# Performance work log

Measured on AMD Instinct MI355X. Metric: run time of the kernel, lower is better.

The kernel has to match this reference:

```python
import jax, jax.numpy as jnp
import numpy as np
from jax import lax

DWT_SCALE = 0.5
IDWT_SCALE = 1.0
PAD = 2  # (kernel_size-1)//2 for k=5


def haar_dwt(x, s):
    """x: [B,C,H,W] -> (ll, lh, hl, hh) each [B,C,H/2,W/2]. 2x2 Haar, scale s."""
    a = x[..., 0::2, 0::2]
    b = x[..., 0::2, 1::2]
    c = x[..., 1::2, 0::2]
    d = x[..., 1::2, 1::2]
    ll = s * (a + b + c + d)
    lh = s * (a + b - c - d)
    hl = s * (a - b + c - d)
    hh = s * (a - b - c + d)
    return ll, lh, hl, hh


def haar_idwt(ll, lh, hl, hh, s):
    """Inverse of haar_dwt when s_dwt * s_idwt_total = 0.5. Returns [B,C,2H,2W]."""
    a = s * (ll + lh + hl + hh)
    b = s * (ll + lh - hl - hh)
    c = s * (ll - lh + hl - hh)
    d = s * (ll - lh - hl + hh)
    B, C, H2, W2 = ll.shape
    top = jnp.stack([a, b], axis=-1).reshape(B, C, H2, 2 * W2)  # even rows
    bot = jnp.stack([c, d], axis=-1).reshape(B, C, H2, 2 * W2)  # odd rows
    return jnp.stack([top, bot], axis=-2).reshape(B, C, 2 * H2, 2 * W2)


def conv2d(x, w, pad):
    return lax.conv_general_dilated(
        x, w, window_strides=(1, 1), padding=[(pad, pad), (pad, pad)],
        dimension_numbers=("NCHW", "OIHW", "NCHW"))


def setup_inputs() -> dict:
    key = jax.random.key(0)
    kx, k0, k1, k2, kb = jax.random.split(key, 5)
    C, K = 64, 5
    x = jax.random.normal(kx, (8, C, 256, 256), dtype=jnp.float32)
    # kaiming_uniform-ish small init to keep 3-level recursion numerically tame
    scale = 0.02
    w0 = jax.random.normal(k0, (4 * C, 4 * C, K, K), dtype=jnp.float32) * scale
    w1 = jax.random.normal(k1, (4 * C, 4 * C, K, K), dtype=jnp.float32) * scale
    w2 = jax.random.normal(k2, (4 * C, 4 * C, K, K), dtype=jnp.float32) * scale
    bias = jax.random.normal(kb, (C,), dtype=jnp.float32) * 0.01
    return {"x": x, "w0": w0, "w1": w1, "w2": w2, "bias": bias}


def reference(x, w0, w1, w2, bias):
    weights = [w0, w1, w2]
    idwt_s = DWT_SCALE * IDWT_SCALE  # perfect reconstruction pair
    curr = x
    ll_levels, high_levels = [], []
    for w in weights:
        ll, lh, hl, hh = haar_dwt(curr, DWT_SCALE)
        curr = ll  # pre-conv LL feeds the next level
        B, C, H2, W2 = ll.shape
        stacked = jnp.stack([ll, lh, hl, hh], axis=2).reshape(B, 4 * C, H2, W2)
        y = conv2d(stacked, w, PAD)  # [B, 4*Co, H2, W2]
        y = y.reshape(B, -1, 4, H2, W2)
        ll_levels.append(y[:, :, 0])
        high_levels.append(y[:, :, 1:])
    next_ll = jnp.zeros_like(ll_levels[-1])
    for ll_t, h_t in zip(reversed(ll_levels), reversed(high_levels)):
        ll = ll_t + next_ll
        next_ll = haar_idwt(ll, h_t[:, :, 0], h_t[:, :, 1], h_t[:, :, 2], idwt_s)
    return next_ll + bias.reshape(1, -1, 1, 1)
```

## Files before the change

kernel.cpp:

```cpp
#include <hip/hip_runtime.h>


typedef unsigned short u16;
typedef __attribute__((ext_vector_type(8))) __bf16 bf16x8;
typedef __attribute__((ext_vector_type(4))) float f32x4;

__device__ __forceinline__ u16 f2bf(float f) {
  union { float f; unsigned u; } v; v.f = f;
  unsigned r = v.u + 0x7fffu + ((v.u >> 16) & 1u);
  return (u16)(r >> 16);
}
__device__ __forceinline__ float bf2f(u16 u) {
  union { unsigned u; float f; } v; v.u = ((unsigned)u) << 16;
  return v.f;
}

typedef const unsigned int __attribute__((address_space(1)))* gas1_t;
typedef unsigned int __attribute__((address_space(3)))* gas3_t;
__device__ __forceinline__ void gload16(const void* g, void* l) {
  __builtin_amdgcn_global_load_lds((gas1_t)g, (gas3_t)l, 16, 0, 0);
}

__global__ void k_wtrans(const float* __restrict__ w, u16* __restrict__ wb) {
  int co = blockIdx.x;
  int ci = threadIdx.x;
  const float* src = w + ((long)co * 256 + ci) * 25;
  float v[25];
#pragma unroll
  for (int tp = 0; tp < 25; ++tp) v[tp] = src[tp];
#pragma unroll
  for (int tp = 0; tp < 25; ++tp)
    wb[((long)tp * 256 + co) * 256 + ci] = f2bf(v[tp]);
}

__global__ void k_border(u16* __restrict__ st, int B_, int H2, int W2) {
  int PW = W2 + 4;
  int npix = 4 * PW + 4 * H2;
  int gid = blockIdx.x * blockDim.x + threadIdx.x;
  int pid = gid >> 6, lane = gid & 63;
  if (pid >= B_ * npix) return;
  int b = pid / npix, p = pid % npix;
  int row, col;
  if (p < 2 * PW) { row = p / PW; col = p % PW; }
  else if (p < 4 * PW) { int q = p - 2 * PW; row = H2 + 2 + q / PW; col = q % PW; }
  else { int q = p - 4 * PW; row = 2 + (q >> 2); int c4 = q & 3; col = (c4 < 2) ? c4 : W2 + c4; }
  long base = (((long)b * (H2 + 4) + row) * PW + col) * 256 + lane * 4;
  *(ushort4*)(st + base) = make_ushort4(0, 0, 0, 0);
}

__global__ void k_dwt(const float* __restrict__ in, u16* __restrict__ st,
                      float* __restrict__ ll, int B_, int H2, int W2) {
  int idx = blockIdx.x * blockDim.x + threadIdx.x;
  int W2h = W2 >> 1;
  int total = B_ * 64 * H2 * W2h;
  if (idx >= total) return;
  int w2h = idx % W2h; int t2 = idx / W2h;
  int h2 = t2 % H2; t2 /= H2;
  int c = t2 % 64; int b = t2 / 64;
  int w2 = w2h * 2;
  const float* r0 = in + (((long)(b * 64 + c) * (2 * H2) + 2 * h2) * (2 * W2)) + 2 * w2;
  const float* r1 = r0 + 2 * W2;
  float4 tp = *(const float4*)r0;
  float4 bt = *(const float4*)r1;
  float ll0 = 0.5f * (tp.x + tp.y + bt.x + bt.y);
  float lh0 = 0.5f * (tp.x + tp.y - bt.x - bt.y);
  float hl0 = 0.5f * (tp.x - tp.y + bt.x - bt.y);
  float hh0 = 0.5f * (tp.x - tp.y - bt.x + bt.y);
  float ll1 = 0.5f * (tp.z + tp.w + bt.z + bt.w);
  float lh1 = 0.5f * (tp.z + tp.w - bt.z - bt.w);
  float hl1 = 0.5f * (tp.z - tp.w + bt.z - bt.w);
  float hh1 = 0.5f * (tp.z - tp.w - bt.z + bt.w);
  long sbase = (((long)b * (H2 + 4) + (h2 + 2)) * (W2 + 4) + (w2 + 2)) * 256 + 4 * c;
  *(ushort4*)(st + sbase)       = make_ushort4(f2bf(ll0), f2bf(lh0), f2bf(hl0), f2bf(hh0));
  *(ushort4*)(st + sbase + 256) = make_ushort4(f2bf(ll1), f2bf(lh1), f2bf(hl1), f2bf(hh1));
  long lbase = (((long)(b * 64 + c) * H2) + h2) * W2 + w2;
  *(float2*)(ll + lbase) = make_float2(ll0, ll1);
}

__global__ __launch_bounds__(512, 2) void k_conv8(
    const u16* __restrict__ st, const u16* __restrict__ wt, u16* __restrict__ out,
    int H2, int W2, int ktot, int nsplit) {
  __shared__ __align__(16) char smem[131072];
  const int t = threadIdx.x;
  const int lane = t & 63;
  const int wv = t >> 6;
  const int wm = wv >> 2, wn = wv & 3;
  const int nwg = gridDim.x;
  const int bid = blockIdx.x;
  const int lb = (bid & 7) * (nwg >> 3) + (bid >> 3);
  const int m0 = lb * 256;
  const int PW = W2 + 4;
  const int spl = blockIdx.y;
  const int kk0 = (spl * ktot) / nsplit;
  const int kk1 = ((spl + 1) * ktot) / nsplit;
  const long Mrows = (long)nwg * 256;
  u16* yo = out + (long)spl * Mrows * 256;

  const int trow = t >> 3;
  const int srcci = ((t & 7) ^ (trow & 7)) * 8;
  const char* baseA[4];
#pragma unroll
  for (int u = 0; u < 4; ++u) {
    int m = m0 + u * 64 + trow;
    int w = m % W2; int q = m / W2;
    int hh = q % H2; int b = q / H2;
    long sp = ((long)(b * (H2 + 4) + hh + 2) * PW + (w + 2));
    baseA[u] = (const char*)(st + sp * 256 + srcci);
  }
  const char* baseB0 = (const char*)(wt + trow * 256 + srcci);

  f32x4 acc[8][4];
#pragma unroll
  for (int i = 0; i < 8; ++i)
#pragma unroll
    for (int j = 0; j < 4; ++j) acc[i][j] = f32x4{0.f, 0.f, 0.f, 0.f};

  const int kq = (lane >> 4) * 16;
  const int sw = (lane & 7) << 4;
  int va0 = (wm * 128 + (lane & 15)) * 128 + (kq ^ sw);
  int va1 = (wm * 128 + (lane & 15)) * 128 + ((64 + kq) ^ sw);
  int vb0 = 32768 + (wn * 64 + (lane & 15)) * 128 + (kq ^ sw);
  int vb1 = 32768 + (wn * 64 + (lane & 15)) * 128 + ((64 + kq) ^ sw);

  bf16x8 a0[4][2], a1[4][2], b0[2][2], b1[2][2];

  auto offsets = [&](int kk, long& oA, long& oB) {
    int tap = kk >> 2, cic = kk & 3;
    int dy = tap / 5 - 2, dx = tap % 5 - 2;
    oA = ((long)(dy * PW + dx) * 256 + cic * 64) * 2;
    oB = ((long)tap * 65536 + cic * 64) * 2;
  };
  auto stageA4 = [&](long off, int dsto) {
    char* d = smem + dsto + wv * 1024;
#pragma unroll
    for (int u = 0; u < 4; ++u) gload16(baseA[u] + off, d + u * 8192);
  };
  auto stageB4 = [&](long off, int dsto) {
    char* d = smem + dsto + 32768 + wv * 1024;
#pragma unroll
    for (int u = 0; u < 4; ++u) gload16(baseB0 + u * 32768 + off, d + u * 8192);
  };

#define LDA0 { _Pragma("unroll") for (int i = 0; i < 4; ++i) {       \
    a0[i][0] = *(const bf16x8*)(smem + va0 + i * 2048);              \
    a0[i][1] = *(const bf16x8*)(smem + va1 + i * 2048); } }
#define LDA1 { _Pragma("unroll") for (int i = 0; i < 4; ++i) {       \
    a1[i][0] = *(const bf16x8*)(smem + va0 + 8192 + i * 2048);       \
    a1[i][1] = *(const bf16x8*)(smem + va1 + 8192 + i * 2048); } }
#define LDB0 { _Pragma("unroll") for (int j = 0; j < 2; ++j) {       \
    b0[j][0] = *(const bf16x8*)(smem + vb0 + j * 2048);              \
    b0[j][1] = *(const bf16x8*)(smem + vb1 + j * 2048); } }
#define LDB1 { _Pragma("unroll") for (int j = 0; j < 2; ++j) {       \
    b1[j][0] = *(const bf16x8*)(smem + vb0 + 4096 + j * 2048);       \
    b1[j][1] = *(const bf16x8*)(smem + vb1 + 4096 + j * 2048); } }
#define MMQ(A, B, IB, JB)                                                     \
  _Pragma("unroll") for (int i = 0; i < 4; ++i)                               \
  _Pragma("unroll") for (int j = 0; j < 2; ++j)                               \
  _Pragma("unroll") for (int k = 0; k < 2; ++k)                               \
    acc[(IB) + i][(JB) + j] = __builtin_amdgcn_mfma_f32_16x16x32_bf16(        \
        A[i][k], B[j][k], acc[(IB) + i][(JB) + j], 0, 0, 0);

  long oA, oB;
  offsets(kk0, oA, oB);
  stageA4(oA, 0); stageB4(oB, 0);
  offsets(kk0 + 1, oA, oB);
  stageA4(oA, 65536); stageB4(oB, 65536);
  asm volatile("s_waitcnt vmcnt(8)" ::: "memory");
  __builtin_amdgcn_s_barrier();
  LDA0 LDB0

  int curo = 0;
  for (int kt = kk0; kt < kk1; ++kt) {
    const bool stg = (kt + 2) < kk1;
    const bool rd1 = (kt + 1) < kk1;
    LDA1 LDB1
    va0 ^= 65536; va1 ^= 65536; vb0 ^= 65536; vb1 ^= 65536;
    __builtin_amdgcn_s_barrier();
    asm volatile("s_waitcnt lgkmcnt(12)" ::: "memory");
    __builtin_amdgcn_sched_barrier(0);
    __builtin_amdgcn_s_setprio(1);
    MMQ(a0, b0, 0, 0)
    __builtin_amdgcn_s_setprio(0);
    __builtin_amdgcn_s_barrier();
    asm volatile("s_waitcnt lgkmcnt(4)" ::: "memory");
    __builtin_amdgcn_sched_barrier(0);
    __builtin_amdgcn_s_setprio(1);
    MMQ(a1, b0, 4, 0)
    __builtin_amdgcn_s_setprio(0);
    if (rd1) { asm volatile("s_waitcnt vmcnt(0)" ::: "memory"); }
    __builtin_amdgcn_s_barrier();
    asm volatile("s_waitcnt lgkmcnt(0)" ::: "memory");
    __builtin_amdgcn_sched_barrier(0);
    __builtin_amdgcn_s_setprio(1);
    MMQ(a1, b1, 4, 2)
    __builtin_amdgcn_s_setprio(0);
    if (rd1) { LDB0 }
    if (stg) { offsets(kt + 2, oA, oB); stageA4(oA, curo); }
    __builtin_amdgcn_s_barrier();
    __builtin_amdgcn_s_setprio(1);
    MMQ(a0, b1, 0, 2)
    __builtin_amdgcn_s_setprio(0);
    if (stg) { stageB4(oB, curo); }
    if (rd1) { LDA0 }
    curo ^= 65536;
  }
#undef MMQ
#undef LDA0
#undef LDA1
#undef LDB0
#undef LDB1

#pragma unroll
  for (int i = 0; i < 8; ++i) {
    int mloc = m0 + wm * 128 + i * 16 + (lane >> 4) * 4;
#pragma unroll
    for (int j = 0; j < 4; ++j) {
      int nloc = wn * 64 + j * 16 + (lane & 15);
#pragma unroll
      for (int r = 0; r < 4; ++r)
        yo[(long)(mloc + r) * 256 + nloc] = f2bf(acc[i][j][r]);
    }
  }
}

__global__ void k_red(const u16* __restrict__ p, u16* __restrict__ y, long n, int ns) {
  long i = ((long)blockIdx.x * 256 + threadIdx.x) * 4;
  if (i >= n) return;
  float s0 = 0.f, s1 = 0.f, s2 = 0.f, s3 = 0.f;
  for (int k = 0; k < ns; ++k) {
    ushort4 v = *(const ushort4*)(p + (long)k * n + i);
    s0 += bf2f(v.x); s1 += bf2f(v.y); s2 += bf2f(v.z); s3 += bf2f(v.w);
  }
  *(ushort4*)(y + i) = make_ushort4(f2bf(s0), f2bf(s1), f2bf(s2), f2bf(s3));
}

__global__ void k_idwt(const u16* __restrict__ y, const float* __restrict__ nll,
                       float* __restrict__ out, const float* __restrict__ bias,
                       int B_, int H2, int W2) {
  int idx = blockIdx.x * blockDim.x + threadIdx.x;
  int W2h = W2 >> 1;
  int total = B_ * 64 * H2 * W2h;
  if (idx >= total) return;
  int w2h = idx % W2h; int t2 = idx / W2h;
  int h2 = t2 % H2; t2 /= H2;
  int c = t2 % 64; int b = t2 / 64;
  int w2 = w2h * 2;
  long ybase = (((long)b * H2 + h2) * W2 + w2) * 256 + 4 * c;
  ushort4 q0 = *(const ushort4*)(y + ybase);
  ushort4 q1 = *(const ushort4*)(y + ybase + 256);
  float llv0 = bf2f(q0.x), lh0 = bf2f(q0.y), hl0 = bf2f(q0.z), hh0 = bf2f(q0.w);
  float llv1 = bf2f(q1.x), lh1 = bf2f(q1.y), hl1 = bf2f(q1.z), hh1 = bf2f(q1.w);
  if (nll) {
    float2 nv = *(const float2*)(nll + (((long)(b * 64 + c) * H2 + h2) * W2 + w2));
    llv0 += nv.x; llv1 += nv.y;
  }
  float bv = bias ? bias[c] : 0.f;
  float a0 = 0.5f * (llv0 + lh0 + hl0 + hh0) + bv;
  float b0 = 0.5f * (llv0 + lh0 - hl0 - hh0) + bv;
  float c0 = 0.5f * (llv0 - lh0 + hl0 - hh0) + bv;
  float d0 = 0.5f * (llv0 - lh0 - hl0 + hh0) + bv;
  float a1 = 0.5f * (llv1 + lh1 + hl1 + hh1) + bv;
  float b1 = 0.5f * (llv1 + lh1 - hl1 - hh1) + bv;
  float c1 = 0.5f * (llv1 - lh1 + hl1 - hh1) + bv;
  float d1 = 0.5f * (llv1 - lh1 - hl1 + hh1) + bv;
  long obase = (((long)(b * 64 + c) * (2 * H2) + 2 * h2) * (2 * W2)) + 2 * w2;
  *(float4*)(out + obase)          = make_float4(a0, b0, a1, b1);
  *(float4*)(out + obase + 2 * W2) = make_float4(c0, d0, c1, d1);
}

constexpr size_t WBF_SZ1 = 25ull * 256 * 256 * 2;
constexpr size_t OFF_WBF = 0;
constexpr size_t OFF_S0  = 3 * WBF_SZ1;
constexpr size_t S0_SZ   = 8ull * 132 * 132 * 256 * 2;
constexpr size_t REL_S1 = 0;
constexpr size_t S1_SZ  = 8ull * 68 * 68 * 256 * 2;
constexpr size_t REL_L1 = REL_S1 + S1_SZ;
constexpr size_t L1_SZ  = 8ull * 64 * 64 * 64 * 4;
constexpr size_t REL_S2 = REL_L1 + L1_SZ;
constexpr size_t S2_SZ  = 8ull * 36 * 36 * 256 * 2;
constexpr size_t REL_Y1 = REL_S2 + S2_SZ;
constexpr size_t Y1_SZ  = 8ull * 64 * 64 * 256 * 2;
constexpr size_t REL_Y2 = REL_Y1 + Y1_SZ;
constexpr size_t Y2_SZ  = 8ull * 32 * 32 * 256 * 2;
constexpr size_t REL_N2 = REL_Y2 + Y2_SZ;
constexpr size_t N2_SZ  = 8ull * 64 * 64 * 64 * 4;
constexpr size_t REL_L2 = REL_N2 + N2_SZ;
constexpr size_t OFF_L0 = OFF_S0 + S0_SZ;
constexpr size_t OFF_Y0 = OFF_L0 + 8ull * 64 * 128 * 128 * 4;

extern "C" void kernel_launch(void* const* d_in, const int* in_sizes, int n_in,
                              void* d_out, int out_size, void* d_ws, size_t ws_size,
                              hipStream_t stream) {
  const float* x    = (const float*)d_in[0];
  const float* w0   = (const float*)d_in[1];
  const float* w1   = (const float*)d_in[2];
  const float* w2   = (const float*)d_in[3];
  const float* bias = (const float*)d_in[4];
  float* out = (float*)d_out;
  char* ws = (char*)d_ws;

  u16* wbf0 = (u16*)(ws + OFF_WBF);
  u16* wbf1 = (u16*)(ws + OFF_WBF + WBF_SZ1);
  u16* wbf2 = (u16*)(ws + OFF_WBF + 2 * WBF_SZ1);
  u16* s0 = (u16*)(ws + OFF_S0);
  u16* s1 = (u16*)(ws + OFF_S0 + REL_S1);
  float* l1 = (float*)(ws + OFF_S0 + REL_L1);
  u16* s2 = (u16*)(ws + OFF_S0 + REL_S2);
  u16* y1 = (u16*)(ws + OFF_S0 + REL_Y1);
  u16* y2 = (u16*)(ws + OFF_S0 + REL_Y2);
  float* n2 = (float*)(ws + OFF_S0 + REL_N2);
  float* l2 = (float*)(ws + OFF_S0 + REL_L2);
  float* l0 = (float*)(ws + OFF_L0);
  u16* P   = (u16*)(ws + OFF_L0);
  float* n1 = (float*)(ws + OFF_L0);
  u16* y0 = (u16*)(ws + OFF_Y0);

  k_wtrans<<<256, 256, 0, stream>>>(w0, wbf0);
  k_wtrans<<<256, 256, 0, stream>>>(w1, wbf1);
  k_wtrans<<<256, 256, 0, stream>>>(w2, wbf2);

  k_border<<<2080, 256, 0, stream>>>(s0, 8, 128, 128);
  k_dwt<<<16384, 256, 0, stream>>>(x, s0, l0, 8, 128, 128);
  k_conv8<<<dim3(512, 1), 512, 0, stream>>>(s0, wbf0, y0, 128, 128, 100, 1);

  k_border<<<1056, 256, 0, stream>>>(s1, 8, 64, 64);
  k_border<<<544, 256, 0, stream>>>(s2, 8, 32, 32);

  k_dwt<<<4096, 256, 0, stream>>>(l0, s1, l1, 8, 64, 64);
  k_conv8<<<dim3(128, 2), 512, 0, stream>>>(s1, wbf1, P, 64, 64, 100, 2);
  k_red<<<8192, 256, 0, stream>>>(P, y1, 8388608L, 2);

  k_dwt<<<1024, 256, 0, stream>>>(l1, s2, l2, 8, 32, 32);
  k_conv8<<<dim3(32, 8), 512, 0, stream>>>(s2, wbf2, P, 32, 32, 100, 8);
  k_red<<<2048, 256, 0, stream>>>(P, y2, 2097152L, 8);

  k_idwt<<<1024, 256, 0, stream>>>(y2, nullptr, n2, nullptr, 8, 32, 32);
  k_idwt<<<4096, 256, 0, stream>>>(y1, n2, n1, nullptr, 8, 64, 64);
  k_idwt<<<16384, 256, 0, stream>>>(y0, n1, out, bias, 8, 128, 128);
}
```

Baseline: 632.7 us.

## Fuse split-K reduction into IDWT, coalesce DWT/IDWT via LDS, merge weight transposes

Folds the split-K partial-sum reduction kernels into the inverse-DWT kernels, dropping the intermediate y1/y2 buffers and two launches. The DWT and IDWT kernels are restructured so each block handles a row segment across all channels, staging channel-interleaved bf16 data in LDS to get coalesced 16-byte global accesses. The three weight-transpose launches are merged into one grid. The workspace layout is reshuffled to reuse buffers, which risks aliasing if lifetimes overlap.

Measured after the change: 721.2 us. +14.0%, slower.

```diff
diff --git a/kernel.cpp b/kernel.cpp
--- a/kernel.cpp
+++ b/kernel.cpp
@@ -3,6 +3,7 @@
 
 typedef unsigned short u16;
 typedef __attribute__((ext_vector_type(8))) __bf16 bf16x8;
+typedef __attribute__((ext_vector_type(8))) unsigned short us8;
 typedef __attribute__((ext_vector_type(4))) float f32x4;
 
 __device__ __forceinline__ u16 f2bf(float f) {
@@ -21,7 +22,11 @@
   __builtin_amdgcn_global_load_lds((gas1_t)g, (gas3_t)l, 16, 0, 0);
 }
 
-__global__ void k_wtrans(const float* __restrict__ w, u16* __restrict__ wb) {
+__global__ void k_wtrans3(const float* __restrict__ wa, const float* __restrict__ wb_,
+                          const float* __restrict__ wc, u16* __restrict__ oa,
+                          u16* __restrict__ ob, u16* __restrict__ oc) {
+  const float* w = (blockIdx.y == 0) ? wa : (blockIdx.y == 1) ? wb_ : wc;
+  u16* o = (blockIdx.y == 0) ? oa : (blockIdx.y == 1) ? ob : oc;
   int co = blockIdx.x;
   int ci = threadIdx.x;
   const float* src = w + ((long)co * 256 + ci) * 25;
@@ -30,7 +35,7 @@
   for (int tp = 0; tp < 25; ++tp) v[tp] = src[tp];
 #pragma unroll
   for (int tp = 0; tp < 25; ++tp)
-    wb[((long)tp * 256 + co) * 256 + ci] = f2bf(v[tp]);
+    o[((long)tp * 256 + co) * 256 + ci] = f2bf(v[tp]);
 }
 
 __global__ void k_border(u16* __restrict__ st, int B_, int H2, int W2) {
@@ -48,33 +53,51 @@
   *(ushort4*)(st + base) = make_ushort4(0, 0, 0, 0);
 }
 
-__global__ void k_dwt(const float* __restrict__ in, u16* __restrict__ st,
-                      float* __restrict__ ll, int B_, int H2, int W2) {
-  int idx = blockIdx.x * blockDim.x + threadIdx.x;
-  int W2h = W2 >> 1;
-  int total = B_ * 64 * H2 * W2h;
-  if (idx >= total) return;
-  int w2h = idx % W2h; int t2 = idx / W2h;
-  int h2 = t2 % H2; t2 /= H2;
-  int c = t2 % 64; int b = t2 / 64;
-  int w2 = w2h * 2;
-  const float* r0 = in + (((long)(b * 64 + c) * (2 * H2) + 2 * h2) * (2 * W2)) + 2 * w2;
+template <int NCOLS>
+__global__ __launch_bounds__(256) void k_dwtT(const float* __restrict__ in,
+                                              u16* __restrict__ st, float* __restrict__ ll,
+                                              int B_, int H2, int W2, int nch) {
+  __shared__ u16 lds16[NCOLS * 256];
+  int blk = blockIdx.x;
+  int cw = blk % nch; int rest = blk / nch;
+  int h2 = rest % H2; int b = rest / H2;
+  int t = threadIdx.x;
+  int c = t >> 2, g = t & 3;
+  constexpr int NC4 = NCOLS / 4;
+  constexpr int NPAIR = NC4 / 2;
+
+  const float* r0 = in + (((long)(b * 64 + c) * (2 * H2) + 2 * h2) * (2 * W2)) + 2 * (cw * NCOLS + g * NC4);
   const float* r1 = r0 + 2 * W2;
-  float4 tp = *(const float4*)r0;
-  float4 bt = *(const float4*)r1;
-  float ll0 = 0.5f * (tp.x + tp.y + bt.x + bt.y);
-  float lh0 = 0.5f * (tp.x + tp.y - bt.x - bt.y);
-  float hl0 = 0.5f * (tp.x - tp.y + bt.x - bt.y);
-  float hh0 = 0.5f * (tp.x - tp.y - bt.x + bt.y);
-  float ll1 = 0.5f * (tp.z + tp.w + bt.z + bt.w);
-  float lh1 = 0.5f * (tp.z + tp.w - bt.z - bt.w);
-  float hl1 = 0.5f * (tp.z - tp.w + bt.z - bt.w);
-  float hh1 = 0.5f * (tp.z - tp.w - bt.z + bt.w);
-  long sbase = (((long)b * (H2 + 4) + (h2 + 2)) * (W2 + 4) + (w2 + 2)) * 256 + 4 * c;
-  *(ushort4*)(st + sbase)       = make_ushort4(f2bf(ll0), f2bf(lh0), f2bf(hl0), f2bf(hh0));
-  *(ushort4*)(st + sbase + 256) = make_ushort4(f2bf(ll1), f2bf(lh1), f2bf(hl1), f2bf(hh1));
-  long lbase = (((long)(b * 64 + c) * H2) + h2) * W2 + w2;
-  *(float2*)(ll + lbase) = make_float2(ll0, ll1);
+  float llv[NC4];
+#pragma unroll
+  for (int j = 0; j < NPAIR; ++j) {
+    float4 tp = *(const float4*)(r0 + 4 * j);
+    float4 bt = *(const float4*)(r1 + 4 * j);
+    float ll0 = 0.5f * (tp.x + tp.y + bt.x + bt.y);
+    float lh0 = 0.5f * (tp.x + tp.y - bt.x - bt.y);
+    float hl0 = 0.5f * (tp.x - tp.y + bt.x - bt.y);
+    float hh0 = 0.5f * (tp.x - tp.y - bt.x + bt.y);
+    float ll1 = 0.5f * (tp.z + tp.w + bt.z + bt.w);
+    float lh1 = 0.5f * (tp.z + tp.w - bt.z - bt.w);
+    float hl1 = 0.5f * (tp.z - tp.w + bt.z - bt.w);
+    float hh1 = 0.5f * (tp.z - tp.w - bt.z + bt.w);
+    int w = g * NC4 + 2 * j;
+    *(ushort4*)(lds16 + w * 256 + 4 * c)       = make_ushort4(f2bf(ll0), f2bf(lh0), f2bf(hl0), f2bf(hh0));
+    *(ushort4*)(lds16 + (w + 1) * 256 + 4 * c) = make_ushort4(f2bf(ll1), f2bf(lh1), f2bf(hl1), f2bf(hh1));
+    llv[2 * j] = ll0; llv[2 * j + 1] = ll1;
+  }
+  float* lp = ll + (((long)(b * 64 + c) * H2 + h2) * W2 + cw * NCOLS + g * NC4);
+#pragma unroll
+  for (int j = 0; j < NC4; j += 4)
+    *(float4*)(lp + j) = make_float4(llv[j], llv[j + 1], llv[j + 2], llv[j + 3]);
+  __syncthreads();
+  u16* dst = st + (((long)b * (H2 + 4) + (h2 + 2)) * (W2 + 4) + 2 + cw * NCOLS) * 256;
+  constexpr int NVEC = NCOLS / 8;
+#pragma unroll
+  for (int i = 0; i < NVEC; ++i) {
+    int eo = (i * 256 + t) * 8;
+    *(us8*)(dst + eo) = *(const us8*)(lds16 + eo);
+  }
 }
 
 __global__ __launch_bounds__(512, 2) void k_conv8(
@@ -223,70 +246,74 @@
   }
 }
 
-__global__ void k_red(const u16* __restrict__ p, u16* __restrict__ y, long n, int ns) {
-  long i = ((long)blockIdx.x * 256 + threadIdx.x) * 4;
-  if (i >= n) return;
-  float s0 = 0.f, s1 = 0.f, s2 = 0.f, s3 = 0.f;
-  for (int k = 0; k < ns; ++k) {
-    ushort4 v = *(const ushort4*)(p + (long)k * n + i);
-    s0 += bf2f(v.x); s1 += bf2f(v.y); s2 += bf2f(v.z); s3 += bf2f(v.w);
-  }
-  *(ushort4*)(y + i) = make_ushort4(f2bf(s0), f2bf(s1), f2bf(s2), f2bf(s3));
-}
-
-__global__ void k_idwt(const u16* __restrict__ y, const float* __restrict__ nll,
-                       float* __restrict__ out, const float* __restrict__ bias,
-                       int B_, int H2, int W2) {
-  int idx = blockIdx.x * blockDim.x + threadIdx.x;
-  int W2h = W2 >> 1;
-  int total = B_ * 64 * H2 * W2h;
-  if (idx >= total) return;
-  int w2h = idx % W2h; int t2 = idx / W2h;
-  int h2 = t2 % H2; t2 /= H2;
-  int c = t2 % 64; int b = t2 / 64;
-  int w2 = w2h * 2;
-  long ybase = (((long)b * H2 + h2) * W2 + w2) * 256 + 4 * c;
-  ushort4 q0 = *(const ushort4*)(y + ybase);
-  ushort4 q1 = *(const ushort4*)(y + ybase + 256);
-  float llv0 = bf2f(q0.x), lh0 = bf2f(q0.y), hl0 = bf2f(q0.z), hh0 = bf2f(q0.w);
-  float llv1 = bf2f(q1.x), lh1 = bf2f(q1.y), hl1 = bf2f(q1.z), hh1 = bf2f(q1.w);
-  if (nll) {
-    float2 nv = *(const float2*)(nll + (((long)(b * 64 + c) * H2 + h2) * W2 + w2));
-    llv0 += nv.x; llv1 += nv.y;
-  }
+template <int NCOLS>
+__global__ __launch_bounds__(256) void k_idwtT(const u16* __restrict__ P, long psz, int ns,
+                                               const float* __restrict__ nll,
+                                               const float* __restrict__ bias,
+                                               float* __restrict__ out,
+                                               int B_, int H2, int W2, int nch) {
+  __shared__ u16 lds16[NCOLS * 256];
+  int blk = blockIdx.x;
+  int cw = blk % nch; int rest = blk / nch;
+  int h2 = rest % H2; int b = rest / H2;
+  int t = threadIdx.x;
+  long span = (((long)b * H2 + h2) * W2 + cw * NCOLS) * 256;
+  constexpr int NVEC = NCOLS / 8;
+#pragma unroll
+  for (int i = 0; i < NVEC; ++i) {
+    int eo = (i * 256 + t) * 8;
+    float s[8] = {0.f, 0.f, 0.f, 0.f, 0.f, 0.f, 0.f, 0.f};
+    for (int k = 0; k < ns; ++k) {
+      us8 v = *(const us8*)(P + (long)k * psz + span + eo);
+#pragma unroll
+      for (int e = 0; e < 8; ++e) s[e] += bf2f(v[e]);
+    }
+    us8 o;
+#pragma unroll
+    for (int e = 0; e < 8; ++e) o[e] = f2bf(s[e]);
+    *(us8*)(lds16 + eo) = o;
+  }
+  __syncthreads();
+  int c = t >> 2, g = t & 3;
+  constexpr int NC4 = NCOLS / 4;
   float bv = bias ? bias[c] : 0.f;
-  float a0 = 0.5f * (llv0 + lh0 + hl0 + hh0) + bv;
-  float b0 = 0.5f * (llv0 + lh0 - hl0 - hh0) + bv;
-  float c0 = 0.5f * (llv0 - lh0 + hl0 - hh0) + bv;
-  float d0 = 0.5f * (llv0 - lh0 - hl0 + hh0) + bv;
-  float a1 = 0.5f * (llv1 + lh1 + hl1 + hh1) + bv;
-  float b1 = 0.5f * (llv1 + lh1 - hl1 - hh1) + bv;
-  float c1 = 0.5f * (llv1 - lh1 + hl1 - hh1) + bv;
-  float d1 = 0.5f * (llv1 - lh1 - hl1 + hh1) + bv;
-  long obase = (((long)(b * 64 + c) * (2 * H2) + 2 * h2) * (2 * W2)) + 2 * w2;
-  *(float4*)(out + obase)          = make_float4(a0, b0, a1, b1);
-  *(float4*)(out + obase + 2 * W2) = make_float4(c0, d0, c1, d1);
+  const float* np = nll ? (nll + (((long)(b * 64 + c) * H2 + h2) * W2 + cw * NCOLS)) : nullptr;
+  float* r0 = out + (((long)(b * 64 + c) * (2 * H2) + 2 * h2) * (2 * W2)) + 2 * (cw * NCOLS);
+  float* r1 = r0 + 2 * W2;
+#pragma unroll
+  for (int j = 0; j < NC4; j += 2) {
+    int w = g * NC4 + j;
+    ushort4 q0 = *(const ushort4*)(lds16 + w * 256 + 4 * c);
+    ushort4 q1 = *(const ushort4*)(lds16 + (w + 1) * 256 + 4 * c);
+    float llv0 = bf2f(q0.x), lh0 = bf2f(q0.y), hl0 = bf2f(q0.z), hh0 = bf2f(q0.w);
+    float llv1 = bf2f(q1.x), lh1 = bf2f(q1.y), hl1 = bf2f(q1.z), hh1 = bf2f(q1.w);
+    if (np) { llv0 += np[w]; llv1 += np[w + 1]; }
+    float a0 = 0.5f * (llv0 + lh0 + hl0 + hh0) + bv;
+    float b0 = 0.5f * (llv0 + lh0 - hl0 - hh0) + bv;
+    float c0 = 0.5f * (llv0 - lh0 + hl0 - hh0) + bv;
+    float d0 = 0.5f * (llv0 - lh0 - hl0 + hh0) + bv;
+    float a1 = 0.5f * (llv1 + lh1 + hl1 + hh1) + bv;
+    float b1 = 0.5f * (llv1 + lh1 - hl1 - hh1) + bv;
+    float c1 = 0.5f * (llv1 - lh1 + hl1 - hh1) + bv;
+    float d1 = 0.5f * (llv1 - lh1 - hl1 + hh1) + bv;
+    *(float4*)(r0 + 2 * w) = make_float4(a0, b0, a1, b1);
+    *(float4*)(r1 + 2 * w) = make_float4(c0, d0, c1, d1);
+  }
 }
 
 constexpr size_t WBF_SZ1 = 25ull * 256 * 256 * 2;
 constexpr size_t OFF_WBF = 0;
 constexpr size_t OFF_S0  = 3 * WBF_SZ1;
 constexpr size_t S0_SZ   = 8ull * 132 * 132 * 256 * 2;
+constexpr size_t OFF_L0  = OFF_S0 + S0_SZ;
+constexpr size_t OFF_Y0  = OFF_L0 + 8ull * 64 * 128 * 128 * 4;
 constexpr size_t REL_S1 = 0;
-constexpr size_t S1_SZ  = 8ull * 68 * 68 * 256 * 2;
-constexpr size_t REL_L1 = REL_S1 + S1_SZ;
-constexpr size_t L1_SZ  = 8ull * 64 * 64 * 64 * 4;
-constexpr size_t REL_S2 = REL_L1 + L1_SZ;
-constexpr size_t S2_SZ  = 8ull * 36 * 36 * 256 * 2;
-constexpr size_t REL_Y1 = REL_S2 + S2_SZ;
-constexpr size_t Y1_SZ  = 8ull * 64 * 64 * 256 * 2;
-constexpr size_t REL_Y2 = REL_Y1 + Y1_SZ;
-constexpr size_t Y2_SZ  = 8ull * 32 * 32 * 256 * 2;
-constexpr size_t REL_N2 = REL_Y2 + Y2_SZ;
-constexpr size_t N2_SZ  = 8ull * 64 * 64 * 64 * 4;
-constexpr size_t REL_L2 = REL_N2 + N2_SZ;
-constexpr size_t OFF_L0 = OFF_S0 + S0_SZ;
-constexpr size_t OFF_Y0 = OFF_L0 + 8ull * 64 * 128 * 128 * 4;
+constexpr size_t REL_L1 = 8ull * 68 * 68 * 256 * 2;
+constexpr size_t REL_S2 = REL_L1 + 8ull * 64 * 64 * 64 * 4;
+constexpr size_t REL_P2 = REL_S2 + 8ull * 36 * 36 * 256 * 2;
+constexpr size_t REL_N2 = 0;
+constexpr size_t REL_N1 = 8ull * 64 * 64 * 64 * 4;
+constexpr size_t REL_L2 = 0;
 
 extern "C" void kernel_launch(void* const* d_in, const int* in_sizes, int n_in,
                               void* d_out, int out_size, void* d_ws, size_t ws_size,
@@ -302,39 +329,34 @@
   u16* wbf0 = (u16*)(ws + OFF_WBF);
   u16* wbf1 = (u16*)(ws + OFF_WBF + WBF_SZ1);
   u16* wbf2 = (u16*)(ws + OFF_WBF + 2 * WBF_SZ1);
-  u16* s0 = (u16*)(ws + OFF_S0);
-  u16* s1 = (u16*)(ws + OFF_S0 + REL_S1);
+  u16* s0   = (u16*)(ws + OFF_S0);
+  u16* s1   = (u16*)(ws + OFF_S0 + REL_S1);
   float* l1 = (float*)(ws + OFF_S0 + REL_L1);
-  u16* s2 = (u16*)(ws + OFF_S0 + REL_S2);
-  u16* y1 = (u16*)(ws + OFF_S0 + REL_Y1);
-  u16* y2 = (u16*)(ws + OFF_S0 + REL_Y2);
+  u16* s2   = (u16*)(ws + OFF_S0 + REL_S2);
+  u16* P2   = (u16*)(ws + OFF_S0 + REL_P2);
   float* n2 = (float*)(ws + OFF_S0 + REL_N2);
+  float* n1 = (float*)(ws + OFF_S0 + REL_N1);
   float* l2 = (float*)(ws + OFF_S0 + REL_L2);
   float* l0 = (float*)(ws + OFF_L0);
-  u16* P   = (u16*)(ws + OFF_L0);
-  float* n1 = (float*)(ws + OFF_L0);
-  u16* y0 = (u16*)(ws + OFF_Y0);
-
-  k_wtrans<<<256, 256, 0, stream>>>(w0, wbf0);
-  k_wtrans<<<256, 256, 0, stream>>>(w1, wbf1);
-  k_wtrans<<<256, 256, 0, stream>>>(w2, wbf2);
+  u16* P1   = (u16*)(ws + OFF_L0);
+  u16* y0   = (u16*)(ws + OFF_Y0);
+
+  k_wtrans3<<<dim3(256, 3), 256, 0, stream>>>(w0, w1, w2, wbf0, wbf1, wbf2);
 
   k_border<<<2080, 256, 0, stream>>>(s0, 8, 128, 128);
-  k_dwt<<<16384, 256, 0, stream>>>(x, s0, l0, 8, 128, 128);
+  k_dwtT<64><<<2048, 256, 0, stream>>>(x, s0, l0, 8, 128, 128, 2);
   k_conv8<<<dim3(512, 1), 512, 0, stream>>>(s0, wbf0, y0, 128, 128, 100, 1);
 
   k_border<<<1056, 256, 0, stream>>>(s1, 8, 64, 64);
   k_border<<<544, 256, 0, stream>>>(s2, 8, 32, 32);
 
-  k_dwt<<<4096, 256, 0, stream>>>(l0, s1, l1, 8, 64, 64);
-  k_conv8<<<dim3(128, 2), 512, 0, stream>>>(s1, wbf1, P, 64, 64, 100, 2);
-  k_red<<<8192, 256, 0, stream>>>(P, y1, 8388608L, 2);
-
-  k_dwt<<<1024, 256, 0, stream>>>(l1, s2, l2, 8, 32, 32);
-  k_conv8<<<dim3(32, 8), 512, 0, stream>>>(s2, wbf2, P, 32, 32, 100, 8);
-  k_red<<<2048, 256, 0, stream>>>(P, y2, 2097152L, 8);
-
-  k_idwt<<<1024, 256, 0, stream>>>(y2, nullptr, n2, nullptr, 8, 32, 32);
-  k_idwt<<<4096, 256, 0, stream>>>(y1, n2, n1, nullptr, 8, 64, 64);
-  k_idwt<<<16384, 256, 0, stream>>>(y0, n1, out, bias, 8, 128, 128);
-}
+  k_dwtT<64><<<512, 256, 0, stream>>>(l0, s1, l1, 8, 64, 64, 1);
+  k_conv8<<<dim3(128, 2), 512, 0, stream>>>(s1, wbf1, P1, 64, 64, 100, 2);
+
+  k_dwtT<32><<<256, 256, 0, stream>>>(l1, s2, l2, 8, 32, 32, 1);
+  k_conv8<<<dim3(32, 8), 512, 0, stream>>>(s2, wbf2, P2, 32, 32, 100, 8);
+
+  k_idwtT<32><<<256, 256, 0, stream>>>(P2, 2097152L, 8, nullptr, nullptr, n2, 8, 32, 32, 1);
+  k_idwtT<64><<<512, 256, 0, stream>>>(P1, 8388608L, 2, n2, nullptr, n1, 8, 64, 64, 1);
+  k_idwtT<64><<<2048, 256, 0, stream>>>(y0, 33554432L, 1, n1, bias, out, 8, 128, 128, 2);
+}
```
